# Kernel tuning notes

Measured on AMD Instinct MI355X. Metric: run time of the kernel, lower is better.

## Reference

```python
import jax, jax.numpy as jnp
import numpy as np

ALPHA = 0.3
BETA = 0.3


def _dema(x, alpha, beta):
    # x: [B, T, C]; 2-state linear recurrence over time implemented with lax.scan
    s0 = x[:, 0, :]                       # [B, C]
    b0 = x[:, 1, :] - s0                  # [B, C]

    def step(carry, xt):
        s_prev, b = carry
        s = alpha * xt + (1.0 - alpha) * (s_prev + b)
        b_new = beta * (s - s_prev) + (1.0 - beta) * b
        return (s, b_new), s

    xs = jnp.moveaxis(x[:, 1:, :], 1, 0)  # [T-1, B, C] for scan over time
    _, ss = jax.lax.scan(step, (s0, b0), xs)
    ma = jnp.concatenate([s0[:, None, :], jnp.moveaxis(ss, 0, 1)], axis=1)  # [B, T, C]
    return ma


def setup_inputs() -> dict:
    key = jax.random.key(0)
    x = jax.random.normal(key, (32, 2048, 512), dtype=jnp.float32)
    return {"x": x}


def reference(x):
    ma = _dema(x, ALPHA, BETA)
    res = x - ma
    return (res, ma)
```

## Files before the change

### kernel.cpp

```cpp
#include <hip/hip_runtime.h>

#define B_   32
#define T_   2048
#define C_   512
#define S_   (B_ * C_)
#define NC_  64
#define L_   (T_ / NC_)
#define NQ_  (S_ / 4)
#define TOTAL_ ((size_t)B_ * T_ * C_)

struct M2 { double m00, m01, m10, m11; };
constexpr M2 mmul(M2 a, M2 b) {
  return { a.m00*b.m00 + a.m01*b.m10, a.m00*b.m01 + a.m01*b.m11,
           a.m10*b.m00 + a.m11*b.m10, a.m10*b.m01 + a.m11*b.m11 };
}
constexpr M2 mpow(M2 a, int n) {
  M2 r{1.0, 0.0, 0.0, 1.0};
  for (int i = 0; i < n; ++i) r = mmul(r, a);
  return r;
}
constexpr double dALPHA = 0.3, dBETA = 0.3;
constexpr M2 M1{1.0 - dALPHA, 1.0 - dALPHA,
                -dALPHA * dBETA, dBETA * (1.0 - dALPHA) + (1.0 - dBETA)};
constexpr M2 ML = mpow(M1, L_);
constexpr float ML00 = (float)ML.m00, ML01 = (float)ML.m01;
constexpr float ML10 = (float)ML.m10, ML11 = (float)ML.m11;

__device__ __forceinline__ void step1(float& s, float& b, float x) {
  const float A = 0.3f, Bt = 0.3f;
  float sp = s;
  s = A * x + (1.0f - A) * (sp + b);
  b = Bt * (s - sp) + (1.0f - Bt) * b;
}
__device__ __forceinline__ void step4(float4& s, float4& b, const float4 x) {
  step1(s.x, b.x, x.x);
  step1(s.y, b.y, x.y);
  step1(s.z, b.z, x.z);
  step1(s.w, b.w, x.w);
}

__global__ __launch_bounds__(256) void dema_pass1(const float* __restrict__ x,
                                                  float* __restrict__ stA) {
  int tid = blockIdx.x * 256 + threadIdx.x;
  int j = tid >> 12;
  int q = tid & (NQ_ - 1);
  int b = q >> 7;
  int c = (q & 127) << 2;
  const float4* xp = reinterpret_cast<const float4*>(
      x + ((size_t)b * T_ + (size_t)j * L_) * C_ + c);
  const int STRD = C_ / 4;

  float4 s, bb;
  if (j == 0) {
    float4 x0 = xp[0];
    float4 x1 = xp[STRD];
    s = x0;
    bb = make_float4(x1.x - x0.x, x1.y - x0.y, x1.z - x0.z, x1.w - x0.w);
    #pragma unroll 4
    for (int t = 1; t < L_; ++t) {
      float4 xt = xp[(size_t)t * STRD];
      step4(s, bb, xt);
    }
  } else {
    s = make_float4(0.f, 0.f, 0.f, 0.f);
    bb = make_float4(0.f, 0.f, 0.f, 0.f);
    #pragma unroll 4
    for (int t = 0; t < L_; ++t) {
      float4 xt = xp[(size_t)t * STRD];
      step4(s, bb, xt);
    }
  }
  float* o = stA + 2 * ((size_t)j * S_ + (size_t)b * C_ + c);
  float4* o4 = reinterpret_cast<float4*>(o);
  o4[0] = make_float4(s.x, bb.x, s.y, bb.y);
  o4[1] = make_float4(s.z, bb.z, s.w, bb.w);
}

__global__ __launch_bounds__(256) void dema_pass2(const float2* __restrict__ stA,
                                                  float2* __restrict__ stB) {
  int sid = blockIdx.x * 256 + threadIdx.x;
  float2 run = stA[sid];
  #pragma unroll 8
  for (int j = 1; j < NC_; ++j) {
    float2 v = stA[(size_t)j * S_ + sid];
    stB[(size_t)j * S_ + sid] = run;
    float ns = ML00 * run.x + ML01 * run.y + v.x;
    float nb = ML10 * run.x + ML11 * run.y + v.y;
    run.x = ns; run.y = nb;
  }
}

__global__ __launch_bounds__(256) void dema_pass3(const float* __restrict__ x,
                                                  const float2* __restrict__ stB,
                                                  float* __restrict__ out) {
  int tid = blockIdx.x * 256 + threadIdx.x;
  int j = tid >> 12;
  int q = tid & (NQ_ - 1);
  int b = q >> 7;
  int c = (q & 127) << 2;
  size_t base = ((size_t)b * T_ + (size_t)j * L_) * C_ + c;
  const float4* xp = reinterpret_cast<const float4*>(x + base);
  float4* resp = reinterpret_cast<float4*>(out + base);
  float4* map  = reinterpret_cast<float4*>(out + TOTAL_ + base);
  const int STRD = C_ / 4;

  float4 s, bb;
  int tstart;
  if (j == 0) {
    float4 x0 = xp[0];
    float4 x1 = xp[STRD];
    s = x0;
    bb = make_float4(x1.x - x0.x, x1.y - x0.y, x1.z - x0.z, x1.w - x0.w);
    map[0]  = s;
    resp[0] = make_float4(0.f, 0.f, 0.f, 0.f);
    tstart = 1;
  } else {
    const float4* st = reinterpret_cast<const float4*>(
        stB + (size_t)j * S_ + (size_t)b * C_ + c);
    float4 p0 = st[0];
    float4 p1 = st[1];
    s  = make_float4(p0.x, p0.z, p1.x, p1.z);
    bb = make_float4(p0.y, p0.w, p1.y, p1.w);
    tstart = 0;
  }
  #pragma unroll 4
  for (int t = tstart; t < L_; ++t) {
    float4 xt = xp[(size_t)t * STRD];
    step4(s, bb, xt);
    map[(size_t)t * STRD] = s;
    resp[(size_t)t * STRD] =
        make_float4(xt.x - s.x, xt.y - s.y, xt.z - s.z, xt.w - s.w);
  }
}

extern "C" void kernel_launch(void* const* d_in, const int* in_sizes, int n_in,
                              void* d_out, int out_size, void* d_ws, size_t ws_size,
                              hipStream_t stream) {
  const float* x = (const float*)d_in[0];
  float* out = (float*)d_out;
  float2* stA = (float2*)d_ws;
  float2* stB = stA + (size_t)NC_ * S_;

  dema_pass1<<<dim3(NC_ * NQ_ / 256), dim3(256), 0, stream>>>(x, (float*)stA);
  dema_pass2<<<dim3(S_ / 256), dim3(256), 0, stream>>>(stA, stB);
  dema_pass3<<<dim3(NC_ * NQ_ / 256), dim3(256), 0, stream>>>(x, stB, out);
}
```

Baseline: 407.1 us.

## Fuse three-pass chunked scan into single-pass kernel with decoupled lookback

Replaces the three-kernel chunked scan (local reduce, serial carry propagation, rescan) with one kernel. Blocks take a dynamic ticket, keep their 32 timesteps of x in registers, publish chunk aggregates with atomic flags, and find their incoming state by walking back over earlier chunks' aggregates with accumulated matrix powers. This removes the second read of x and the extra launches, at the cost of heavy register use from caching 32 float4 values, spin-waiting, and an O(chunk index) lookback per block.

```diff
diff --git a/kernel.cpp b/kernel.cpp
--- a/kernel.cpp
+++ b/kernel.cpp
@@ -6,7 +6,8 @@
 #define S_   (B_ * C_)
 #define NC_  64
 #define L_   (T_ / NC_)
-#define NQ_  (S_ / 4)
+#define GPC_ 16
+#define NBLK_ (NC_ * GPC_)
 #define TOTAL_ ((size_t)B_ * T_ * C_)
 
 struct M2 { double m00, m01, m10, m11; };
@@ -39,97 +40,119 @@
   step1(s.w, b.w, x.w);
 }
 
-__global__ __launch_bounds__(256) void dema_pass1(const float* __restrict__ x,
-                                                  float* __restrict__ stA) {
-  int tid = blockIdx.x * 256 + threadIdx.x;
-  int j = tid >> 12;
-  int q = tid & (NQ_ - 1);
-  int b = q >> 7;
-  int c = (q & 127) << 2;
-  const float4* xp = reinterpret_cast<const float4*>(
-      x + ((size_t)b * T_ + (size_t)j * L_) * C_ + c);
+__device__ __forceinline__ void publish2(float2* p, float sv, float bv) {
+  union { float2 f; unsigned long long u; } w;
+  w.f = make_float2(sv, bv);
+  __hip_atomic_store((unsigned long long*)p, w.u,
+                     __ATOMIC_RELAXED, __HIP_MEMORY_SCOPE_AGENT);
+}
+__device__ __forceinline__ float2 readagg(const float2* p) {
+  union { float2 f; unsigned long long u; } w;
+  w.u = __hip_atomic_load((const unsigned long long*)p,
+                          __ATOMIC_RELAXED, __HIP_MEMORY_SCOPE_AGENT);
+  return w.f;
+}
+
+__global__ void zero_ctrl(unsigned int* __restrict__ p, int n) {
+  int i = blockIdx.x * 256 + threadIdx.x;
+  if (i < n) p[i] = 0u;
+}
+
+__global__ __launch_bounds__(256, 2) void dema_fused(
+    const float* __restrict__ x, float* __restrict__ out,
+    float2* __restrict__ stA, unsigned int* __restrict__ flags,
+    unsigned int* __restrict__ ticket) {
+  __shared__ unsigned int s_tau;
+  if (threadIdx.x == 0) s_tau = atomicAdd(ticket, 1u);
+  __syncthreads();
+  const int tau = (int)s_tau;
+  const int c = tau >> 4;
+  const int g = tau & (GPC_ - 1);
+  const int q = g * 256 + (int)threadIdx.x;
+  const int bb = q >> 7;
+  const int ch = (q & 127) << 2;
+  const size_t base = ((size_t)bb * T_ + (size_t)c * L_) * C_ + ch;
+  const float4* xp = reinterpret_cast<const float4*>(x + base);
   const int STRD = C_ / 4;
 
-  float4 s, bb;
-  if (j == 0) {
-    float4 x0 = xp[0];
-    float4 x1 = xp[STRD];
-    s = x0;
-    bb = make_float4(x1.x - x0.x, x1.y - x0.y, x1.z - x0.z, x1.w - x0.w);
-    #pragma unroll 4
+  float4 xv[L_];
+  #pragma unroll
+  for (int t = 0; t < L_; ++t) xv[t] = xp[(size_t)t * STRD];
+
+  float4 s, b;
+  if (c == 0) {
+    s = xv[0];
+    b = make_float4(xv[1].x - xv[0].x, xv[1].y - xv[0].y,
+                    xv[1].z - xv[0].z, xv[1].w - xv[0].w);
+    #pragma unroll
+    for (int t = 1; t < L_; ++t) step4(s, b, xv[t]);
+  } else {
+    s = make_float4(0.f, 0.f, 0.f, 0.f);
+    b = make_float4(0.f, 0.f, 0.f, 0.f);
+    #pragma unroll
+    for (int t = 0; t < L_; ++t) step4(s, b, xv[t]);
+  }
+
+  float2* ap = stA + (size_t)c * S_ + (size_t)bb * C_ + ch;
+  publish2(ap + 0, s.x, b.x);
+  publish2(ap + 1, s.y, b.y);
+  publish2(ap + 2, s.z, b.z);
+  publish2(ap + 3, s.w, b.w);
+  __syncthreads();
+  if (threadIdx.x == 0) {
+    __threadfence();
+    __hip_atomic_store(&flags[tau], 1u, __ATOMIC_RELEASE,
+                       __HIP_MEMORY_SCOPE_AGENT);
+  }
+
+  float4* resp = reinterpret_cast<float4*>(out + base);
+  float4* map  = reinterpret_cast<float4*>(out + TOTAL_ + base);
+
+  if (c == 0) {
+    s = xv[0];
+    b = make_float4(xv[1].x - xv[0].x, xv[1].y - xv[0].y,
+                    xv[1].z - xv[0].z, xv[1].w - xv[0].w);
+    map[0]  = s;
+    resp[0] = make_float4(0.f, 0.f, 0.f, 0.f);
+    #pragma unroll
     for (int t = 1; t < L_; ++t) {
-      float4 xt = xp[(size_t)t * STRD];
-      step4(s, bb, xt);
+      float4 xt = xv[t];
+      step4(s, b, xt);
+      map[(size_t)t * STRD] = s;
+      resp[(size_t)t * STRD] =
+          make_float4(xt.x - s.x, xt.y - s.y, xt.z - s.z, xt.w - s.w);
     }
   } else {
-    s = make_float4(0.f, 0.f, 0.f, 0.f);
-    bb = make_float4(0.f, 0.f, 0.f, 0.f);
-    #pragma unroll 4
+    float2 v0 = {0.f, 0.f}, v1 = {0.f, 0.f}, v2 = {0.f, 0.f}, v3 = {0.f, 0.f};
+    float p00 = 1.f, p01 = 0.f, p10 = 0.f, p11 = 1.f;
+    for (int j = c - 1; j >= 0; --j) {
+      const unsigned int* f = &flags[(j << 4) | g];
+      while (__hip_atomic_load(f, __ATOMIC_ACQUIRE,
+                               __HIP_MEMORY_SCOPE_AGENT) == 0u)
+        __builtin_amdgcn_s_sleep(4);
+      const float2* jp = stA + (size_t)j * S_ + (size_t)bb * C_ + ch;
+      float2 a0 = readagg(jp + 0);
+      float2 a1 = readagg(jp + 1);
+      float2 a2 = readagg(jp + 2);
+      float2 a3 = readagg(jp + 3);
+      v0.x += p00 * a0.x + p01 * a0.y;  v0.y += p10 * a0.x + p11 * a0.y;
+      v1.x += p00 * a1.x + p01 * a1.y;  v1.y += p10 * a1.x + p11 * a1.y;
+      v2.x += p00 * a2.x + p01 * a2.y;  v2.y += p10 * a2.x + p11 * a2.y;
+      v3.x += p00 * a3.x + p01 * a3.y;  v3.y += p10 * a3.x + p11 * a3.y;
+      float n00 = ML00 * p00 + ML01 * p10, n01 = ML00 * p01 + ML01 * p11;
+      float n10 = ML10 * p00 + ML11 * p10, n11 = ML10 * p01 + ML11 * p11;
+      p00 = n00; p01 = n01; p10 = n10; p11 = n11;
+    }
+    s = make_float4(v0.x, v1.x, v2.x, v3.x);
+    b = make_float4(v0.y, v1.y, v2.y, v3.y);
+    #pragma unroll
     for (int t = 0; t < L_; ++t) {
-      float4 xt = xp[(size_t)t * STRD];
-      step4(s, bb, xt);
+      float4 xt = xv[t];
+      step4(s, b, xt);
+      map[(size_t)t * STRD] = s;
+      resp[(size_t)t * STRD] =
+          make_float4(xt.x - s.x, xt.y - s.y, xt.z - s.z, xt.w - s.w);
     }
-  }
-  float* o = stA + 2 * ((size_t)j * S_ + (size_t)b * C_ + c);
-  float4* o4 = reinterpret_cast<float4*>(o);
-  o4[0] = make_float4(s.x, bb.x, s.y, bb.y);
-  o4[1] = make_float4(s.z, bb.z, s.w, bb.w);
-}
-
-__global__ __launch_bounds__(256) void dema_pass2(const float2* __restrict__ stA,
-                                                  float2* __restrict__ stB) {
-  int sid = blockIdx.x * 256 + threadIdx.x;
-  float2 run = stA[sid];
-  #pragma unroll 8
-  for (int j = 1; j < NC_; ++j) {
-    float2 v = stA[(size_t)j * S_ + sid];
-    stB[(size_t)j * S_ + sid] = run;
-    float ns = ML00 * run.x + ML01 * run.y + v.x;
-    float nb = ML10 * run.x + ML11 * run.y + v.y;
-    run.x = ns; run.y = nb;
-  }
-}
-
-__global__ __launch_bounds__(256) void dema_pass3(const float* __restrict__ x,
-                                                  const float2* __restrict__ stB,
-                                                  float* __restrict__ out) {
-  int tid = blockIdx.x * 256 + threadIdx.x;
-  int j = tid >> 12;
-  int q = tid & (NQ_ - 1);
-  int b = q >> 7;
-  int c = (q & 127) << 2;
-  size_t base = ((size_t)b * T_ + (size_t)j * L_) * C_ + c;
-  const float4* xp = reinterpret_cast<const float4*>(x + base);
-  float4* resp = reinterpret_cast<float4*>(out + base);
-  float4* map  = reinterpret_cast<float4*>(out + TOTAL_ + base);
-  const int STRD = C_ / 4;
-
-  float4 s, bb;
-  int tstart;
-  if (j == 0) {
-    float4 x0 = xp[0];
-    float4 x1 = xp[STRD];
-    s = x0;
-    bb = make_float4(x1.x - x0.x, x1.y - x0.y, x1.z - x0.z, x1.w - x0.w);
-    map[0]  = s;
-    resp[0] = make_float4(0.f, 0.f, 0.f, 0.f);
-    tstart = 1;
-  } else {
-    const float4* st = reinterpret_cast<const float4*>(
-        stB + (size_t)j * S_ + (size_t)b * C_ + c);
-    float4 p0 = st[0];
-    float4 p1 = st[1];
-    s  = make_float4(p0.x, p0.z, p1.x, p1.z);
-    bb = make_float4(p0.y, p0.w, p1.y, p1.w);
-    tstart = 0;
-  }
-  #pragma unroll 4
-  for (int t = tstart; t < L_; ++t) {
-    float4 xt = xp[(size_t)t * STRD];
-    step4(s, bb, xt);
-    map[(size_t)t * STRD] = s;
-    resp[(size_t)t * STRD] =
-        make_float4(xt.x - s.x, xt.y - s.y, xt.z - s.z, xt.w - s.w);
   }
 }
 
@@ -139,9 +162,11 @@
   const float* x = (const float*)d_in[0];
   float* out = (float*)d_out;
   float2* stA = (float2*)d_ws;
-  float2* stB = stA + (size_t)NC_ * S_;
+  unsigned int* flags =
+      (unsigned int*)((char*)d_ws + (size_t)NC_ * S_ * sizeof(float2));
 
-  dema_pass1<<<dim3(NC_ * NQ_ / 256), dim3(256), 0, stream>>>(x, (float*)stA);
-  dema_pass2<<<dim3(S_ / 256), dim3(256), 0, stream>>>(stA, stB);
-  dema_pass3<<<dim3(NC_ * NQ_ / 256), dim3(256), 0, stream>>>(x, stB, out);
+  zero_ctrl<<<dim3((NBLK_ + 1 + 255) / 256), dim3(256), 0, stream>>>(
+      flags, NBLK_ + 1);
+  dema_fused<<<dim3(NBLK_), dim3(256), 0, stream>>>(
+      x, out, stA, flags, flags + NBLK_);
 }
```

Result: slower. 1.499 ms (+268.2%).
